# Kernel optimization log

Measured on AMD Instinct MI355X. Metric: run time of the kernel, lower is better.

## Reference

```python
import jax, jax.numpy as jnp
import numpy as np

WS = 8          # window_size
OWS = 12        # overlap_win_size = int(8*0.5)+8
PAD = 2         # (OWS-WS)//2
HEADS = 6
DH = 16         # dim_head
INNER = HEADS * DH  # 96
SCALE = DH ** -0.5


def rel_to_abs(x):
    # x: (b, l, m) with m = 2*r - 1
    b, l, m = x.shape
    r = (m + 1) // 2
    x = jnp.concatenate([x, jnp.zeros((b, l, 1), x.dtype)], axis=2)
    flat = x.reshape(b, l * (m + 1))
    flat = jnp.concatenate([flat, jnp.zeros((b, m - l), x.dtype)], axis=1)
    final = flat.reshape(b, l + 1, m)[:, :l, m - r:]
    return final  # (b, l, r)


def relative_logits_1d(q, rel_k):
    # q: (B, X, Y, d), rel_k: (2r-1, d)
    B, X, Y, _ = q.shape
    r = (rel_k.shape[0] + 1) // 2
    logits = jnp.einsum('bxyd,rd->bxyr', q, rel_k)           # (B, X, Y, 2r-1)
    logits = rel_to_abs(logits.reshape(B * X, Y, -1)).reshape(B, X, Y, r)
    logits = jnp.broadcast_to(logits[:, :, None], (B, X, r, Y, r))  # b x i y j
    return logits


def rel_pos_emb(q, rel_height, rel_width):
    # q: (B, WS*WS, d) -> bias (B, WS*WS, OWS*OWS)
    B, _, d = q.shape
    qg = q.reshape(B, WS, WS, d)
    lw = relative_logits_1d(qg, rel_width)                   # (B, x, i, y, j)
    lw = lw.transpose(0, 1, 3, 2, 4).reshape(B, WS * WS, OWS * OWS)  # b (x y) (i j)
    lh = relative_logits_1d(qg.transpose(0, 2, 1, 3), rel_height)    # (B, y, i, x, j) roles swapped
    lh = lh.transpose(0, 3, 1, 4, 2).reshape(B, WS * WS, OWS * OWS)  # b (y x) (j i)
    return lw + lh


def unfold_windows(t, nh, nw):
    # torch nn.Unfold(kernel=OWS, stride=WS, padding=PAD) then
    # rearrange 'b (c j) i -> (b i) j c' -> (b*nh*nw, OWS*OWS, C)
    b, C, _, _ = t.shape
    tp = jnp.pad(t, ((0, 0), (0, 0), (PAD, PAD), (PAD, PAD)))
    ridx = (jnp.arange(nh) * WS)[:, None] + jnp.arange(OWS)   # (nh, OWS)
    cidx = (jnp.arange(nw) * WS)[:, None] + jnp.arange(OWS)   # (nw, OWS)
    p = tp[:, :, ridx, :]            # (b, C, nh, OWS, Wp)
    p = p[:, :, :, :, cidx]          # (b, C, nh, OWS, nw, OWS)
    p = p.transpose(0, 2, 4, 3, 5, 1)  # (b, nh, nw, OWS, OWS, C)
    return p.reshape(b * nh * nw, OWS * OWS, C)


def split_heads(t):
    # (B, n, heads*dh) -> (B*heads, n, dh)
    B, n, _ = t.shape
    return t.reshape(B, n, HEADS, DH).transpose(0, 2, 1, 3).reshape(B * HEADS, n, DH)


def setup_inputs() -> dict:
    key = jax.random.key(0)
    k = jax.random.split(key, 5)
    x = jax.random.normal(k[0], (2, 96, 256, 256), jnp.float32)
    qkv_w = jax.random.normal(k[1], (288, 96), jnp.float32) * 0.05
    qkv_b = jnp.zeros((288,), jnp.float32)
    proj_w = jax.random.normal(k[2], (96, 96), jnp.float32) * 0.05
    proj_b = jnp.zeros((96,), jnp.float32)
    rel_height = jax.random.normal(k[3], (23, 16), jnp.float32) * SCALE
    rel_width = jax.random.normal(k[4], (23, 16), jnp.float32) * SCALE
    return {"x": x, "qkv_w": qkv_w, "qkv_b": qkv_b, "proj_w": proj_w,
            "proj_b": proj_b, "rel_height": rel_height, "rel_width": rel_width}


def reference(x, qkv_w, qkv_b, proj_w, proj_b, rel_height, rel_width):
    b, c, h, w = x.shape
    nh, nw = h // WS, w // WS
    qkv = jnp.einsum('oc,bchw->bohw', qkv_w, x) + qkv_b[None, :, None, None]
    qs, ks, vs = jnp.split(qkv, 3, axis=1)  # each (b, INNER, h, w)
    # queries: non-overlapping windows 'b c (h p1) (w p2) -> (b h w) (p1 p2) c'
    qs = qs.reshape(b, INNER, nh, WS, nw, WS).transpose(0, 2, 4, 3, 5, 1)
    qs = qs.reshape(b * nh * nw, WS * WS, INNER)
    ks = unfold_windows(ks, nh, nw)  # (b*nh*nw, OWS*OWS, INNER)
    vs = unfold_windows(vs, nh, nw)
    qs, ks, vs = map(split_heads, (qs, ks, vs))  # (B*heads, n, DH)
    qs = qs * SCALE
    attn = jnp.einsum('bqd,bkd->bqk', qs, ks)
    attn = attn + rel_pos_emb(qs, rel_height, rel_width)
    attn = jax.nn.softmax(attn, axis=-1)
    out = jnp.einsum('bqk,bkd->bqd', attn, vs)  # (b*nh*nw*heads, WS*WS, DH)
    out = out.reshape(b, nh, nw, HEADS, WS, WS, DH)
    out = out.transpose(0, 3, 6, 1, 4, 2, 5).reshape(b, INNER, h, w)
    out = jnp.einsum('oc,bchw->bohw', proj_w, out) + proj_b[None, :, None, None]
    return out
```

## Files before the change

### kernel.cpp

```cpp
#include <hip/hip_runtime.h>
#include <hip/hip_bf16.h>


typedef __attribute__((ext_vector_type(8))) short bf16x8;
typedef __attribute__((ext_vector_type(4))) float f32x4;
typedef __attribute__((ext_vector_type(4))) unsigned u32x4;

__device__ __forceinline__ f32x4 mfma16(bf16x8 a, bf16x8 b, f32x4 c) {
  return __builtin_amdgcn_mfma_f32_16x16x32_bf16(a, b, c, 0, 0, 0);
}
__device__ __forceinline__ short f2b(float f) {
  unsigned u = __builtin_bit_cast(unsigned, f);
  unsigned r = u + 0x7fffu + ((u >> 16) & 1u);
  return (short)(r >> 16);
}
__device__ __forceinline__ unsigned cvtpk(float lo, float hi) {
  unsigned r;
  asm("v_cvt_pk_bf16_f32 %0, %1, %2" : "=v"(r) : "v"(lo), "v"(hi));
  return r;
}
__device__ __forceinline__ void splitf(float x, short& h, short& l) {
  unsigned u = __builtin_bit_cast(unsigned, x);
  h = (short)(u >> 16);
  float fh = __builtin_bit_cast(float, u & 0xffff0000u);
  l = f2b(x - fh);
}

#define KPLANE 1081600L
#define QS (0.25f * 1.44269504f)

__global__ __launch_bounds__(256) void prep_kernel(
    const float* __restrict__ qkv_w, const float* __restrict__ proj_w,
    const float* __restrict__ rel_h, const float* __restrict__ rel_w,
    const float* __restrict__ qkv_b,
    short* __restrict__ qwh, short* __restrict__ qwl,
    short* __restrict__ pwh, short* __restrict__ pwl,
    short* __restrict__ rhb, short* __restrict__ rwb,
    float* __restrict__ sbias, short* __restrict__ k_t) {
  int i = blockIdx.x * 256 + threadIdx.x;
  if (i < 288 * 96) {
    float wv = qkv_w[i];
    if (i < 96 * 96) wv *= QS;
    short h, l;
    splitf(wv, h, l);
    qwh[i] = h;
    qwl[i] = l;
  }
  if (i < 96 * 96) {
    short h, l;
    splitf(proj_w[i], h, l);
    pwh[i] = h;
    pwl[i] = l;
  }
  if (i < 368) {
    rhb[i] = f2b(rel_h[i]);
    rwb[i] = f2b(rel_w[i]);
  }
  if (i < 288) sbias[i] = qkv_b[i] * (i < 96 ? QS : 1.0f);
  if (i < 12 * 2064) {
    int plane = i / 2064, r = i - plane * 2064;
    int py, px;
    if (r < 1040) {
      int rowid = r / 260;
      py = (rowid < 2) ? rowid : 256 + rowid;
      px = r - rowid * 260;
    } else {
      int r2 = r - 1040;
      py = 2 + (r2 >> 2);
      int cid = r2 & 3;
      px = (cid < 2) ? cid : 256 + cid;
    }
    bf16x8 z = {0, 0, 0, 0, 0, 0, 0, 0};
    long base = (long)plane * KPLANE + (long)(py * 260 + px) * 16;
    *(bf16x8*)(k_t + base) = z;
    *(bf16x8*)(k_t + base + 8) = z;
  }
}

__global__ __launch_bounds__(256) void qkv_kernel(
    const float* __restrict__ x, const short* __restrict__ qwh,
    const short* __restrict__ qwl, const float* __restrict__ sbias,
    short* __restrict__ q_t, short* __restrict__ k_t,
    short* __restrict__ v_t) {
  const int tid = threadIdx.x;
  const int wave = tid >> 6, lane = tid & 63;
  const int quad = lane >> 4, col = lane & 15;
  const int blk = blockIdx.x;
  const int b = blk >> 8, row = blk & 255;

  const float* xw = x + (((long)b * 96) << 16) + row * 256 + wave * 64 + col;
  bf16x8 bx[4][3];
#pragma unroll
  for (int tile = 0; tile < 4; ++tile)
#pragma unroll
    for (int ks = 0; ks < 3; ++ks) {
      const float* p = xw + tile * 16 + (((long)(ks * 32 + quad * 8)) << 16);
      float v0 = p[0];
      float v1 = p[1L << 16];
      float v2 = p[2L << 16];
      float v3 = p[3L << 16];
      float v4 = p[4L << 16];
      float v5 = p[5L << 16];
      float v6 = p[6L << 16];
      float v7 = p[7L << 16];
      union { unsigned u[4]; bf16x8 w; } t;
      t.u[0] = cvtpk(v0, v1);
      t.u[1] = cvtpk(v2, v3);
      t.u[2] = cvtpk(v4, v5);
      t.u[3] = cvtpk(v6, v7);
      bx[tile][ks] = t.w;
    }

  const short* wbh = qwh + col * 96 + quad * 8;
  const short* wbl = qwl + col * 96 + quad * 8;
  bf16x8 wh[3], wl[3];
#pragma unroll
  for (int ks = 0; ks < 3; ++ks) {
    wh[ks] = *(const bf16x8*)(wbh + ks * 32);
    wl[ks] = *(const bf16x8*)(wbl + ks * 32);
  }

  const long pixb = (long)blk * 256 + wave * 64 + col;
  short* kbase = k_t + (long)b * KPLANE +
                 ((long)((row + 2) * 260 + wave * 64 + col + 2)) * 16 +
                 quad * 4;

#pragma unroll
  for (int t6 = 0; t6 < 18; ++t6) {
    bf16x8 nh[3], nl[3];
    if (t6 < 17) {
#pragma unroll
      for (int ks = 0; ks < 3; ++ks) {
        nh[ks] = *(const bf16x8*)(wbh + (t6 + 1) * 1536 + ks * 32);
        nl[ks] = *(const bf16x8*)(wbl + (t6 + 1) * 1536 + ks * 32);
      }
    }
    f32x4 bv = *(const f32x4*)(sbias + t6 * 16 + quad * 4);
    f32x4 acc[4] = {bv, bv, bv, bv};
#pragma unroll
    for (int ks = 0; ks < 3; ++ks)
#pragma unroll
      for (int tile = 0; tile < 4; ++tile) {
        acc[tile] = mfma16(wh[ks], bx[tile][ks], acc[tile]);
        acc[tile] = mfma16(wl[ks], bx[tile][ks], acc[tile]);
      }
#pragma unroll
    for (int tile = 0; tile < 4; ++tile) {
      unsigned d0 = cvtpk(acc[tile][0], acc[tile][1]);
      unsigned d1 = cvtpk(acc[tile][2], acc[tile][3]);
      if (t6 >= 6 && t6 < 12) {
        short* kp = kbase + (long)(t6 - 6) * (2 * KPLANE) + tile * 256;
        *(unsigned*)kp = d0;
        *(unsigned*)(kp + 2) = d1;
      } else {
        short* plane = (t6 < 6 ? q_t : v_t) +
                       (long)(t6 < 6 ? t6 : t6 - 12) * 2097152 + pixb * 16 +
                       tile * 256 + quad * 4;
        *(unsigned*)plane = d0;
        *(unsigned*)(plane + 2) = d1;
      }
    }
    if (t6 < 17) {
#pragma unroll
      for (int ks = 0; ks < 3; ++ks) {
        wh[ks] = nh[ks];
        wl[ks] = nl[ks];
      }
    }
  }
}

__global__ __launch_bounds__(256) void attn_kernel(
    const short* __restrict__ q_t, const short* __restrict__ k_t,
    const short* __restrict__ v_t, const short* __restrict__ rhb,
    const short* __restrict__ rwb, short* __restrict__ ao) {
  __shared__ __attribute__((aligned(16))) short v_lds[16][168];
  __shared__ __attribute__((aligned(16))) char scratch[4][5376];

  const int orig = blockIdx.x, head = blockIdx.y;
  const int win = ((orig & 7) << 8) | (orig >> 3);
  const int b = win >> 10, wy = (win & 1023) >> 5, wx = win & 31;
  const int y0 = wy * 8 - 2, x0 = wx * 8 - 2;
  const long pb = (long)b << 16;
  const int tid = threadIdx.x;

  if (tid < 160) {
    const int key = tid;
    bool valid = false;
    long pix = 0;
    if (key < 144) {
      int kh = key / 12, kw = key - kh * 12;
      int gy = y0 + kh, gx = x0 + kw;
      valid = ((unsigned)gy < 256u) && ((unsigned)gx < 256u);
      pix = pb + gy * 256 + gx;
    }
    if (valid) {
      const short* src = v_t + (long)head * 2097152 + pix * 16;
      union { bf16x8 v; short s[8]; } u0, u1;
      u0.v = *(const bf16x8*)src;
      u1.v = *(const bf16x8*)(src + 8);
      for (int d = 0; d < 8; ++d) {
        v_lds[d][key] = u0.s[d];
        v_lds[d + 8][key] = u1.s[d];
      }
    } else {
      for (int d = 0; d < 16; ++d) v_lds[d][key] = 0;
    }
  }
  __syncthreads();

  const int wave = tid >> 6, lane = tid & 63;
  const int quad = lane >> 4, col = lane & 15;
  float* Ws = (float*)scratch[wave];
  float* Ht = Ws + 320;
  unsigned* ppd = (unsigned*)scratch[wave];

  const short* qp = q_t + (long)head * 2097152;
  const short* kpb = k_t + (long)(head * 2 + b) * KPLANE;

  bf16x8 qf = {0, 0, 0, 0, 0, 0, 0, 0};
  if (quad < 2) {
    int qg = wave * 16 + col;
    int qy = qg >> 3, qx = qg & 7;
    qf = *(const bf16x8*)(qp + (pb + (wy * 8 + qy) * 256 + wx * 8 + qx) * 16 +
                          quad * 8);
  }

  for (int nt2 = 0; nt2 < 2; ++nt2) {
    int r = nt2 * 16 + col;
    bf16x8 bw = {0, 0, 0, 0, 0, 0, 0, 0}, bh2 = bw;
    if (quad < 2 && r < 23) {
      bw = *(const bf16x8*)(rwb + r * 16 + quad * 8);
      bh2 = *(const bf16x8*)(rhb + r * 16 + quad * 8);
    }
    f32x4 z = {0.f, 0.f, 0.f, 0.f};
    f32x4 aw = mfma16(qf, bw, z);
    f32x4 ahh = mfma16(qf, bh2, z);
    int kh = r - 11 + wave * 2 + (quad >> 1);
#pragma unroll
    for (int r4 = 0; r4 < 4; ++r4) {
      int q = quad * 4 + r4;
      int kw = r - 11 + (q & 7);
      if ((unsigned)kw < 12u) Ws[q * 20 + kw] = aw[r4];
      if ((unsigned)kh < 12u) Ht[q * 20 + kh] = ahh[r4];
    }
  }
  asm volatile("" ::: "memory");

  const f32x4 wv4 = *(const f32x4*)&Ws[col * 20 + quad * 4];
  const f32x4 h0 = *(const f32x4*)&Ht[col * 20];
  const f32x4 h1 = *(const f32x4*)&Ht[col * 20 + 4];
  const f32x4 h2 = *(const f32x4*)&Ht[col * 20 + 8];
  asm volatile("" ::: "memory");

  if (quad < 2) {
    u32x4 z4 = {0u, 0u, 0u, 0u};
    *(u32x4*)(ppd + col * 84 + 72 + quad * 4) = z4;
  }
  asm volatile("" ::: "memory");

  const short* kb =
      kpb + (long)((wy * 8) * 260 + wx * 8 + col) * 16 + quad * 8;
#pragma unroll
  for (int nt = 0; nt < 12; ++nt) {
    bf16x8 kf = *(const bf16x8*)(kb + (long)nt * 4160);
    float hs = nt < 4 ? h0[nt] : (nt < 8 ? h1[nt - 4] : h2[nt - 8]);
    f32x4 acc = wv4 + hs;
    f32x4 L = mfma16(kf, qf, acc);
    unsigned d0 = cvtpk(__builtin_amdgcn_exp2f(L[0]),
                        __builtin_amdgcn_exp2f(L[1]));
    unsigned d1 = cvtpk(__builtin_amdgcn_exp2f(L[2]),
                        __builtin_amdgcn_exp2f(L[3]));
    if (quad < 3) {
      ppd[col * 84 + nt * 6 + quad * 2] = d0;
      ppd[col * 84 + nt * 6 + quad * 2 + 1] = d1;
    }
  }
  asm volatile("" ::: "memory");

  const bf16x8 ones = {0x3F80, 0x3F80, 0x3F80, 0x3F80,
                       0x3F80, 0x3F80, 0x3F80, 0x3F80};
  f32x4 oacc = {0.f, 0.f, 0.f, 0.f}, oaccS = oacc;
#pragma unroll
  for (int ks = 0; ks < 5; ++ks) {
    int base = ks * 4 + quad;
    union { u32x4 u; bf16x8 v; } pu;
    pu.u = *(const u32x4*)(ppd + col * 84 + base * 4);
    bf16x8 vb = *(const bf16x8*)&v_lds[col][ks * 32 + quad * 8];
    oacc = mfma16(pu.v, vb, oacc);
    oaccS = mfma16(pu.v, ones, oaccS);
  }
  for (int r4 = 0; r4 < 4; ++r4) {
    int qg = wave * 16 + quad * 4 + r4;
    int qy = qg >> 3, qx = qg & 7;
    float val = oacc[r4] * __builtin_amdgcn_rcpf(oaccS[r4]);
    ao[(long)head * 2097152 +
       (pb + (wy * 8 + qy) * 256 + wx * 8 + qx) * 16 + col] = f2b(val);
  }
}

__global__ __launch_bounds__(256) void proj_kernel(
    const short* __restrict__ ao, const short* __restrict__ pwh,
    const short* __restrict__ pwl, const float* __restrict__ bias,
    float* __restrict__ out) {
  const int tid = threadIdx.x;
  const int wave = tid >> 6, lane = tid & 63;
  const int quad = lane >> 4, col = lane & 15;
  const int blk = blockIdx.x;
  const int b = blk >> 8;
  const long pix0 = (long)blk * 256 + wave * 64 + col;

  bf16x8 bfr[4][3];
#pragma unroll
  for (int tile = 0; tile < 4; ++tile)
#pragma unroll
    for (int ks = 0; ks < 3; ++ks) {
      int head = 2 * ks + (quad >> 1);
      bfr[tile][ks] =
          *(const bf16x8*)(ao + (long)head * 2097152 +
                           (pix0 + tile * 16) * 16 + (quad & 1) * 8);
    }

  const short* wbh = pwh + col * 96 + quad * 8;
  const short* wbl = pwl + col * 96 + quad * 8;
  bf16x8 ah[3], al[3];
#pragma unroll
  for (int ks = 0; ks < 3; ++ks) {
    ah[ks] = *(const bf16x8*)(wbh + ks * 32);
    al[ks] = *(const bf16x8*)(wbl + ks * 32);
  }
  float* ob = out + (((long)(b * 96 + quad * 4)) << 16) + (blk & 255) * 256 +
              wave * 64 + col;
#pragma unroll
  for (int mt = 0; mt < 6; ++mt) {
    bf16x8 nh[3], nl[3];
    if (mt < 5) {
#pragma unroll
      for (int ks = 0; ks < 3; ++ks) {
        nh[ks] = *(const bf16x8*)(wbh + (mt + 1) * 1536 + ks * 32);
        nl[ks] = *(const bf16x8*)(wbl + (mt + 1) * 1536 + ks * 32);
      }
    }
    f32x4 bv = *(const f32x4*)(bias + mt * 16 + quad * 4);
    f32x4 acc[4] = {bv, bv, bv, bv};
#pragma unroll
    for (int ks = 0; ks < 3; ++ks)
#pragma unroll
      for (int tile = 0; tile < 4; ++tile) {
        acc[tile] = mfma16(ah[ks], bfr[tile][ks], acc[tile]);
        acc[tile] = mfma16(al[ks], bfr[tile][ks], acc[tile]);
      }
    float* obm = ob + ((long)(mt * 16) << 16);
#pragma unroll
    for (int tile = 0; tile < 4; ++tile)
#pragma unroll
      for (int r = 0; r < 4; ++r)
        obm[((long)r << 16) + tile * 16] = acc[tile][r];
    if (mt < 5) {
#pragma unroll
      for (int ks = 0; ks < 3; ++ks) {
        ah[ks] = nh[ks];
        al[ks] = nl[ks];
      }
    }
  }
}

extern "C" void kernel_launch(void* const* d_in, const int* in_sizes, int n_in,
                              void* d_out, int out_size, void* d_ws,
                              size_t ws_size, hipStream_t stream) {
  const float* x = (const float*)d_in[0];
  const float* qkv_w = (const float*)d_in[1];
  const float* qkv_b = (const float*)d_in[2];
  const float* proj_w = (const float*)d_in[3];
  const float* proj_b = (const float*)d_in[4];
  const float* rel_h = (const float*)d_in[5];
  const float* rel_w = (const float*)d_in[6];

  const long NPIXC = 131072L * 96L;
  short* q_t = (short*)d_ws;
  short* k_t = q_t + NPIXC;
  short* v_t = k_t + 12 * KPLANE;
  short* ao = v_t + NPIXC;
  short* qwh = ao + NPIXC;
  short* qwl = qwh + 288 * 96;
  short* pwh = qwl + 288 * 96;
  short* pwl = pwh + 96 * 96;
  short* rhb = pwl + 96 * 96;
  short* rwb = rhb + 368;
  float* sbias = (float*)(rwb + 368);
  float* out = (float*)d_out;

  hipLaunchKernelGGL(prep_kernel, dim3(108), dim3(256), 0, stream, qkv_w,
                     proj_w, rel_h, rel_w, qkv_b, qwh, qwl, pwh, pwl, rhb, rwb,
                     sbias, k_t);
  hipLaunchKernelGGL(qkv_kernel, dim3(512), dim3(256), 0, stream, x, qwh, qwl,
                     sbias, q_t, k_t, v_t);
  hipLaunchKernelGGL(attn_kernel, dim3(2048, 6), dim3(256), 0, stream, q_t,
                     k_t, v_t, rhb, rwb, ao);
  hipLaunchKernelGGL(proj_kernel, dim3(512), dim3(256), 0, stream, ao, pwh,
                     pwl, proj_b, out);
}
```

Before: 205.6 us.

## Shuffle softmax probabilities in registers via permlane swaps instead of LDS

Replaces the LDS round-trip for the exponentiated score tile (write P to per-wave scratch, then reload as the A operand of the PV MFMA) with v_permlane16/32_swap register shuffles that transpose two score tiles directly into operand layout. The QK and PV loops are fused so each step computes two key tiles and feeds them straight into the value MFMA. The V staging is repadded to a 16-wide key row layout (12 valid plus 4 zero) to match the new register layout, and launch bounds now request 8 blocks per CU. This removes LDS traffic and barriers but increases register pressure and relies on the new padded key ordering being correct.

```diff
diff --git a/kernel.cpp b/kernel.cpp
--- a/kernel.cpp
+++ b/kernel.cpp
@@ -18,6 +18,12 @@
   unsigned r;
   asm("v_cvt_pk_bf16_f32 %0, %1, %2" : "=v"(r) : "v"(lo), "v"(hi));
   return r;
+}
+__device__ __forceinline__ void pl16s(unsigned& a, unsigned& b) {
+  asm("v_permlane16_swap_b32 %0, %1" : "+v"(a), "+v"(b));
+}
+__device__ __forceinline__ void pl32s(unsigned& a, unsigned& b) {
+  asm("v_permlane32_swap_b32 %0, %1" : "+v"(a), "+v"(b));
 }
 __device__ __forceinline__ void splitf(float x, short& h, short& l) {
   unsigned u = __builtin_bit_cast(unsigned, x);
@@ -170,12 +176,13 @@
   }
 }
 
-__global__ __launch_bounds__(256) void attn_kernel(
+__global__ __launch_bounds__(256, 8) void attn_kernel(
     const short* __restrict__ q_t, const short* __restrict__ k_t,
     const short* __restrict__ v_t, const short* __restrict__ rhb,
     const short* __restrict__ rwb, short* __restrict__ ao) {
-  __shared__ __attribute__((aligned(16))) short v_lds[16][168];
-  __shared__ __attribute__((aligned(16))) char scratch[4][5376];
+  __shared__ __attribute__((aligned(16))) short v_lds[16][210];
+  __shared__ __attribute__((aligned(16))) float Wt[4][16][20];
+  __shared__ __attribute__((aligned(16))) float Htab[4][16][20];
 
   const int orig = blockIdx.x, head = blockIdx.y;
   const int win = ((orig & 7) << 8) | (orig >> 3);
@@ -184,36 +191,31 @@
   const long pb = (long)b << 16;
   const int tid = threadIdx.x;
 
-  if (tid < 160) {
-    const int key = tid;
-    bool valid = false;
-    long pix = 0;
-    if (key < 144) {
-      int kh = key / 12, kw = key - kh * 12;
-      int gy = y0 + kh, gx = x0 + kw;
-      valid = ((unsigned)gy < 256u) && ((unsigned)gx < 256u);
-      pix = pb + gy * 256 + gx;
-    }
+  if (tid < 192) {
+    const int kh = tid >> 4, kw = tid & 15;
+    const int gy = y0 + kh, gx = x0 + kw;
+    const bool valid =
+        (kw < 12) && ((unsigned)gy < 256u) && ((unsigned)gx < 256u);
     if (valid) {
-      const short* src = v_t + (long)head * 2097152 + pix * 16;
+      const short* src =
+          v_t + (long)head * 2097152 + (pb + gy * 256 + gx) * 16;
       union { bf16x8 v; short s[8]; } u0, u1;
       u0.v = *(const bf16x8*)src;
       u1.v = *(const bf16x8*)(src + 8);
       for (int d = 0; d < 8; ++d) {
-        v_lds[d][key] = u0.s[d];
-        v_lds[d + 8][key] = u1.s[d];
+        v_lds[d][tid] = u0.s[d];
+        v_lds[d + 8][tid] = u1.s[d];
       }
     } else {
-      for (int d = 0; d < 16; ++d) v_lds[d][key] = 0;
+      for (int d = 0; d < 16; ++d) v_lds[d][tid] = 0;
     }
   }
   __syncthreads();
 
   const int wave = tid >> 6, lane = tid & 63;
   const int quad = lane >> 4, col = lane & 15;
-  float* Ws = (float*)scratch[wave];
-  float* Ht = Ws + 320;
-  unsigned* ppd = (unsigned*)scratch[wave];
+  float* Ws = &Wt[wave][0][0];
+  float* Ht = &Htab[wave][0][0];
 
   const short* qp = q_t + (long)head * 2097152;
   const short* kpb = k_t + (long)(head * 2 + b) * KPLANE;
@@ -251,41 +253,41 @@
   const f32x4 h0 = *(const f32x4*)&Ht[col * 20];
   const f32x4 h1 = *(const f32x4*)&Ht[col * 20 + 4];
   const f32x4 h2 = *(const f32x4*)&Ht[col * 20 + 8];
-  asm volatile("" ::: "memory");
-
-  if (quad < 2) {
-    u32x4 z4 = {0u, 0u, 0u, 0u};
-    *(u32x4*)(ppd + col * 84 + 72 + quad * 4) = z4;
-  }
-  asm volatile("" ::: "memory");
 
   const short* kb =
       kpb + (long)((wy * 8) * 260 + wx * 8 + col) * 16 + quad * 8;
-#pragma unroll
-  for (int nt = 0; nt < 12; ++nt) {
-    bf16x8 kf = *(const bf16x8*)(kb + (long)nt * 4160);
-    float hs = nt < 4 ? h0[nt] : (nt < 8 ? h1[nt - 4] : h2[nt - 8]);
-    f32x4 acc = wv4 + hs;
-    f32x4 L = mfma16(kf, qf, acc);
-    unsigned d0 = cvtpk(__builtin_amdgcn_exp2f(L[0]),
-                        __builtin_amdgcn_exp2f(L[1]));
-    unsigned d1 = cvtpk(__builtin_amdgcn_exp2f(L[2]),
-                        __builtin_amdgcn_exp2f(L[3]));
-    if (quad < 3) {
-      ppd[col * 84 + nt * 6 + quad * 2] = d0;
-      ppd[col * 84 + nt * 6 + quad * 2 + 1] = d1;
-    }
-  }
-  asm volatile("" ::: "memory");
-
   const bf16x8 ones = {0x3F80, 0x3F80, 0x3F80, 0x3F80,
                        0x3F80, 0x3F80, 0x3F80, 0x3F80};
   f32x4 oacc = {0.f, 0.f, 0.f, 0.f}, oaccS = oacc;
 #pragma unroll
-  for (int ks = 0; ks < 5; ++ks) {
-    int base = ks * 4 + quad;
+  for (int ks = 0; ks < 6; ++ks) {
+    const int nt0 = 2 * ks, nt1 = 2 * ks + 1;
+    bf16x8 kf0 = *(const bf16x8*)(kb + (long)nt0 * 4160);
+    bf16x8 kf1 = *(const bf16x8*)(kb + (long)nt1 * 4160);
+    float hs0 = nt0 < 4 ? h0[nt0] : (nt0 < 8 ? h1[nt0 - 4] : h2[nt0 - 8]);
+    float hs1 = nt1 < 4 ? h0[nt1] : (nt1 < 8 ? h1[nt1 - 4] : h2[nt1 - 8]);
+    f32x4 a0 = wv4 + hs0, a1 = wv4 + hs1;
+    f32x4 L0 = mfma16(kf0, qf, a0);
+    f32x4 L1 = mfma16(kf1, qf, a1);
+    unsigned X = cvtpk(__builtin_amdgcn_exp2f(L0[0]),
+                       __builtin_amdgcn_exp2f(L0[1]));
+    unsigned Y = cvtpk(__builtin_amdgcn_exp2f(L0[2]),
+                       __builtin_amdgcn_exp2f(L0[3]));
+    unsigned Xp = cvtpk(__builtin_amdgcn_exp2f(L1[0]),
+                        __builtin_amdgcn_exp2f(L1[1]));
+    unsigned Yp = cvtpk(__builtin_amdgcn_exp2f(L1[2]),
+                        __builtin_amdgcn_exp2f(L1[3]));
+    pl16s(X, Y);
+    pl16s(Xp, Yp);
+    pl32s(X, Xp);
+    pl32s(Y, Yp);
+    pl16s(X, Xp);
+    pl16s(Y, Yp);
     union { u32x4 u; bf16x8 v; } pu;
-    pu.u = *(const u32x4*)(ppd + col * 84 + base * 4);
+    pu.u[0] = X;
+    pu.u[1] = Xp;
+    pu.u[2] = (quad & 1) ? 0u : Y;
+    pu.u[3] = (quad & 1) ? 0u : Yp;
     bf16x8 vb = *(const bf16x8*)&v_lds[col][ks * 32 + quad * 8];
     oacc = mfma16(pu.v, vb, oacc);
     oaccS = mfma16(pu.v, ones, oaccS);
```

After: 189.8 us. 7.7% less time.
